# Performance work log

Hardware: AMD Instinct MI355X
Metric: run time of the kernel (lower is better)

Reference implementation:

```python
import jax, jax.numpy as jnp
import numpy as np

EPS = 1e-5

def batchnorm2d(x, w, b):
    # training-mode BN: per-channel stats over (B, H, W), biased variance
    mean = jnp.mean(x, axis=(0, 2, 3), keepdims=True)
    var = jnp.var(x, axis=(0, 2, 3), keepdims=True)
    xn = (x - mean) * jax.lax.rsqrt(var + EPS)
    return xn * w[None, :, None, None] + b[None, :, None, None]

def setup_inputs() -> dict:
    key = jax.random.key(0)
    ks = jax.random.split(key, 12)
    B, C, H, W = 4, 64, 64, 64
    Cq = C // 8
    s = 1.0 / np.sqrt(C)
    return {
        "x": jax.random.normal(ks[0], (B, C, H, W), jnp.float32),
        "Wq": jax.random.normal(ks[1], (Cq, C), jnp.float32) * s,
        "bq": jnp.zeros((Cq,), jnp.float32),
        "Wk": jax.random.normal(ks[2], (Cq, C), jnp.float32) * s,
        "bk": jnp.zeros((Cq,), jnp.float32),
        "Wv": jax.random.normal(ks[3], (C, C), jnp.float32) * s,
        "bv": jnp.zeros((C,), jnp.float32),
        "gamma_p": jax.random.normal(ks[4], (), jnp.float32) * 0.1,
        "bnp_w": jnp.ones((C,), jnp.float32),
        "bnp_b": jnp.zeros((C,), jnp.float32),
        "gamma_c": jax.random.normal(ks[5], (), jnp.float32) * 0.1,
        "bnc_w": jnp.ones((C,), jnp.float32),
        "bnc_b": jnp.zeros((C,), jnp.float32),
    }

def reference(x, Wq, bq, Wk, bk, Wv, bv, gamma_p, bnp_w, bnp_b, gamma_c, bnc_w, bnc_b):
    B, C, H, W = x.shape
    N = H * W
    xf = x.reshape(B, C, N)

    # ---- PAM (position attention) ----
    q = jnp.einsum('dc,bcn->bnd', Wq, xf) + bq  # [B, N, Cq]
    k = jnp.einsum('dc,bcn->bdn', Wk, xf) + bk[None, :, None]  # [B, Cq, N]
    v = jnp.einsum('dc,bcn->bdn', Wv, xf) + bv[None, :, None]  # [B, C, N]
    energy = jnp.einsum('bnd,bdm->bnm', q, k)  # [B, N, N]
    attn = jax.nn.softmax(energy, axis=-1)
    # out[b,c,m] = sum_n v[b,c,n] * attn[m,n]  (bmm(v, attn^T))
    out = jnp.einsum('bcn,bmn->bcm', v, attn).reshape(B, C, H, W)
    out = gamma_p * out
    out = batchnorm2d(out, bnp_w, bnp_b)
    y = out + x  # PAM residual

    # ---- CAM (channel attention) ----
    yf = y.reshape(B, C, N)
    energy_c = jnp.einsum('bcn,bdn->bcd', yf, yf)  # [B, C, C]
    energy_new = jnp.max(energy_c, axis=-1, keepdims=True) - energy_c
    attn_c = jax.nn.softmax(energy_new, axis=-1)
    out_c = jnp.einsum('bcd,bdn->bcn', attn_c, yf).reshape(B, C, H, W)
    out_c = gamma_c * out_c
    out_c = batchnorm2d(out_c, bnc_w, bnc_b)
    return out_c + y  # CAM residual
```

## Files before the change

kernel.cpp:

```cpp
#include <hip/hip_runtime.h>

#define NN 4096
#define EPS 1e-5f

#define Q_OFF   0u
#define K_OFF   131072u
#define V_OFF   262144u
#define O_OFF   1310720u
#define Y_OFF   2359296u
#define OC_OFF  3407872u
#define AT_OFF  4456448u
#define S2_OFF  4472832u
#define PS_OFF  4472960u
#define OP_OFF  4473088u

__global__ __launch_bounds__(256) void proj_kernel(
    const float* __restrict__ x, const float* __restrict__ Wq, const float* __restrict__ bq,
    const float* __restrict__ Wk, const float* __restrict__ bk,
    const float* __restrict__ Wv, const float* __restrict__ bv,
    float* __restrict__ q, float* __restrict__ k, float* __restrict__ v) {
  __shared__ float sWq[8*64], sWk[8*64], sWv[64*64], sbq[8], sbk[8], sbv[64];
  int t = threadIdx.x;
  for (int i = t; i < 512; i += 256) { sWq[i] = Wq[i]; sWk[i] = Wk[i]; }
  for (int i = t; i < 4096; i += 256) sWv[i] = Wv[i];
  if (t < 64) sbv[t] = bv[t];
  if (t < 8) { sbq[t] = bq[t]; sbk[t] = bk[t]; }
  __syncthreads();
  int b = blockIdx.x >> 6;
  int n = ((blockIdx.x & 63) << 6) | (t & 63);
  int cg_ = t >> 6;
  float xv[64];
  #pragma unroll
  for (int c = 0; c < 64; ++c) xv[c] = x[(((b<<6)|c)<<12) | n];
  for (int c = cg_*16; c < cg_*16+16; ++c) {
    float acc = sbv[c];
    #pragma unroll
    for (int c2 = 0; c2 < 64; ++c2) acc += sWv[c*64 + c2] * xv[c2];
    v[(((b<<6)|c)<<12) | n] = acc;
  }
  if (cg_ == 0) {
    #pragma unroll
    for (int d = 0; d < 8; ++d) {
      float acc = sbq[d];
      #pragma unroll
      for (int c = 0; c < 64; ++c) acc += sWq[d*64+c] * xv[c];
      q[(((b<<12)|n)<<3) | d] = acc;
    }
  } else if (cg_ == 1) {
    #pragma unroll
    for (int d = 0; d < 8; ++d) {
      float acc = sbk[d];
      #pragma unroll
      for (int c = 0; c < 64; ++c) acc += sWk[d*64+c] * xv[c];
      k[(((b<<3)|d)<<12) | n] = acc;
    }
  }
}

__global__ __launch_bounds__(256, 4) void attn_kernel(
    const float* __restrict__ q, const float* __restrict__ k,
    const float* __restrict__ v, float* __restrict__ op,
    float* __restrict__ lp, int gsh) {
  __shared__ float kst[64*12];
  __shared__ float vst[64*68];
  __shared__ float pst[64*68];

  const int G    = 1 << gsh;
  const int g    = blockIdx.x & (G - 1);
  const int rest = blockIdx.x >> gsh;
  const int mt   = rest & 63;
  const int b    = rest >> 6;
  const int m0   = mt << 6;
  const int t    = threadIdx.x;

  const int rq = t & 15;
  const int sg = t >> 4;

  float4 qa[4][2];
  #pragma unroll
  for (int r = 0; r < 4; ++r) {
    const float4* qp = (const float4*)&q[(size_t)(((b<<12) | (m0 + (rq<<2) + r)) << 3)];
    qa[r][0] = qp[0]; qa[r][1] = qp[1];
  }

  float lsum[4] = {0.f, 0.f, 0.f, 0.f};
  float av[4][4] = {{0.f}};

  const int span = NN >> gsh;
  const int nbeg = g * span;

  for (int n0 = nbeg; n0 < nbeg + span; n0 += 64) {
    __syncthreads();
    #pragma unroll
    for (int i = t; i < 512; i += 256) {
      int ni = i & 63, d = i >> 6;
      kst[ni*12 + d] = k[(((b<<3)|d)<<12) + n0 + ni];
    }
    #pragma unroll
    for (int i = t; i < 4096; i += 256) {
      int ni = i & 63, c = i >> 6;
      vst[ni*68 + c] = v[(((b<<6)|c)<<12) + n0 + ni];
    }
    __syncthreads();
    #pragma unroll
    for (int j = 0; j < 4; ++j) {
      const int ni = (sg << 2) | j;
      const float4 ka = *(const float4*)&kst[ni*12];
      const float4 kb = *(const float4*)&kst[ni*12 + 4];
      float pj[4];
      #pragma unroll
      for (int r = 0; r < 4; ++r) {
        float s = qa[r][0].x*ka.x + qa[r][0].y*ka.y + qa[r][0].z*ka.z + qa[r][0].w*ka.w
                + qa[r][1].x*kb.x + qa[r][1].y*kb.y + qa[r][1].z*kb.z + qa[r][1].w*kb.w;
        float e = __expf(s);
        pj[r] = e;
        lsum[r] += e;
      }
      *(float4*)&pst[ni*68 + (rq<<2)] = make_float4(pj[0], pj[1], pj[2], pj[3]);
    }
    __syncthreads();
    #pragma unroll 4
    for (int ni = 0; ni < 64; ++ni) {
      const float4 p4 = *(const float4*)&pst[ni*68 + (sg<<2)];
      const float4 v4 = *(const float4*)&vst[ni*68 + (rq<<2)];
      av[0][0] += p4.x*v4.x; av[0][1] += p4.x*v4.y; av[0][2] += p4.x*v4.z; av[0][3] += p4.x*v4.w;
      av[1][0] += p4.y*v4.x; av[1][1] += p4.y*v4.y; av[1][2] += p4.y*v4.z; av[1][3] += p4.y*v4.w;
      av[2][0] += p4.z*v4.x; av[2][1] += p4.z*v4.y; av[2][2] += p4.z*v4.z; av[2][3] += p4.z*v4.w;
      av[3][0] += p4.w*v4.x; av[3][1] += p4.w*v4.y; av[3][2] += p4.w*v4.z; av[3][3] += p4.w*v4.w;
    }
  }
  __syncthreads();
  *(float4*)&pst[sg*68 + (rq<<2)] = make_float4(lsum[0], lsum[1], lsum[2], lsum[3]);
  __syncthreads();
  if (t < 64) {
    float l = 0.f;
    #pragma unroll
    for (int s = 0; s < 16; ++s) l += pst[s*68 + t];
    lp[(((((g<<2)|b)<<6) | mt)<<6) | t] = l;
  }
  float* ob = op + ((size_t)((((g<<2)|b)<<6) | mt) << 12);
  #pragma unroll
  for (int r = 0; r < 4; ++r)
    *(float4*)&ob[((((sg<<2)|r)<<6) | (rq<<2))] =
        make_float4(av[r][0], av[r][1], av[r][2], av[r][3]);
}

__global__ __launch_bounds__(256) void merge_kernel(
    const float* __restrict__ op, const float* __restrict__ lp,
    float* __restrict__ o, float* __restrict__ psums, int G) {
  __shared__ float sm[64*65];
  __shared__ float linv[64];
  const int b = blockIdx.x >> 6, mt = blockIdx.x & 63;
  const int t = threadIdx.x;
  if (t < 64) {
    float l = 0.f;
    for (int g = 0; g < G; ++g)
      l += lp[(((((g<<2)|b)<<6) | mt)<<6) | t];
    linv[t] = 1.f / l;
  }
  __syncthreads();
  for (int i = 0; i < 16; ++i) {
    int idx = (i<<8) + t;
    float s = 0.f;
    for (int g = 0; g < G; ++g)
      s += op[((size_t)((((g<<2)|b)<<6) | mt) << 12) + idx];
    int m = idx >> 6, c = idx & 63;
    sm[c*65 + m] = s * linv[m];
  }
  __syncthreads();
  for (int i = 0; i < 16; ++i) {
    int idx = (i<<8) + t;
    int m = idx & 63, c = idx >> 6;
    float ov = sm[c*65 + m];
    o[(((b<<6)|c)<<12) | (mt<<6) | m] = ov;
    float s1 = ov, s2 = ov*ov;
    #pragma unroll
    for (int off = 32; off; off >>= 1) {
      s1 += __shfl_xor(s1, off, 64);
      s2 += __shfl_xor(s2, off, 64);
    }
    if ((t & 63) == 0) { atomicAdd(&psums[c], s1); atomicAdd(&psums[64+c], s2); }
  }
}

__global__ __launch_bounds__(256) void yg_kernel(
    const float* __restrict__ o, const float* __restrict__ x,
    const float* __restrict__ psums,
    const float* __restrict__ gp, const float* __restrict__ w1, const float* __restrict__ bb1,
    float* __restrict__ y, float* __restrict__ gpart) {
  __shared__ float yt[64*68];
  __shared__ float cf[128];
  const int bi = blockIdx.x;
  const int b = bi >> 6, sp = bi & 63;
  const int t = threadIdx.x;
  const int n0 = sp << 6;
  if (t < 64) {
    float m1 = psums[t] * (1.f/16384.f), m2 = psums[64+t] * (1.f/16384.f);
    float var = m2 - m1*m1;
    float gg = *gp;
    float r = rsqrtf(gg*gg*var + EPS);
    float a = gg * r * w1[t];
    cf[t] = a; cf[64+t] = bb1[t] - m1*a;
  }
  __syncthreads();
  #pragma unroll
  for (int i = 0; i < 16; ++i) {
    int idx = (i<<8) + t;
    int c = idx >> 6, m = idx & 63;
    size_t gi = ((size_t)(((b<<6)|c)<<12)) + n0 + m;
    float yv = o[gi]*cf[c] + cf[64+c] + x[gi];
    yt[c*68 + m] = yv;
    y[gi] = yv;
  }
  __syncthreads();
  {
    int tc = t >> 4, td = t & 15;
    float acc[4][4] = {{0.f}};
    #pragma unroll
    for (int mj = 0; mj < 16; ++mj) {
      float4 ya[4], yb[4];
      #pragma unroll
      for (int r = 0; r < 4; ++r)  ya[r] = *(const float4*)&yt[((tc<<2)+r)*68 + (mj<<2)];
      #pragma unroll
      for (int ss = 0; ss < 4; ++ss) yb[ss] = *(const float4*)&yt[((td<<2)+ss)*68 + (mj<<2)];
      #pragma unroll
      for (int r = 0; r < 4; ++r)
        #pragma unroll
        for (int ss = 0; ss < 4; ++ss)
          acc[r][ss] += ya[r].x*yb[ss].x + ya[r].y*yb[ss].y + ya[r].z*yb[ss].z + ya[r].w*yb[ss].w;
    }
    float* gb = gpart + ((size_t)bi << 12);
    #pragma unroll
    for (int r = 0; r < 4; ++r)
      *(float4*)&gb[(((tc<<2)+r)<<6) | (td<<2)] =
          make_float4(acc[r][0], acc[r][1], acc[r][2], acc[r][3]);
  }
}

__global__ __launch_bounds__(256) void csm_kernel(
    const float* __restrict__ gpart, float* __restrict__ attnc) {
  __shared__ float red[256];
  const int bi = blockIdx.x;
  const int b = bi >> 6, row = bi & 63;
  const int t = threadIdx.x;
  const int d = t & 63, spg = t >> 6;
  float e = 0.f;
  #pragma unroll
  for (int j = 0; j < 16; ++j) {
    int spp = (spg<<4) + j;
    e += gpart[((size_t)((b<<6)|spp) << 12) + (row<<6) + d];
  }
  red[t] = e;
  __syncthreads();
  if (t < 64) {
    float ee = red[t]+red[64+t]+red[128+t]+red[192+t];
    float mn = ee;
    #pragma unroll
    for (int off = 32; off; off >>= 1) mn = fminf(mn, __shfl_xor(mn, off, 64));
    float p = __expf(mn - ee);
    float s = p;
    #pragma unroll
    for (int off = 32; off; off >>= 1) s += __shfl_xor(s, off, 64);
    attnc[(((b<<6)|row)<<6) | t] = p / s;
  }
}

__global__ __launch_bounds__(256) void cam_apply_kernel(
    const float* __restrict__ attn, const float* __restrict__ y,
    float* __restrict__ oc, float* __restrict__ sums) {
  __shared__ float satt[64*68];
  int b = blockIdx.x >> 6;
  int n = ((blockIdx.x & 63) << 6) | (threadIdx.x & 63);
  int cg_ = threadIdx.x >> 6;
  for (int i = threadIdx.x; i < 4096; i += 256)
    satt[(i>>6)*68 + (i&63)] = attn[(b<<12) | i];
  __syncthreads();
  float yv[64];
  #pragma unroll
  for (int d = 0; d < 64; ++d) yv[d] = y[(((b<<6)|d)<<12) | n];
  for (int c = cg_*16; c < cg_*16+16; ++c) {
    float acc = 0.f;
    #pragma unroll
    for (int d4 = 0; d4 < 16; ++d4) {
      float4 avv = *(const float4*)&satt[c*68 + (d4<<2)];
      acc += avv.x*yv[d4*4] + avv.y*yv[d4*4+1] + avv.z*yv[d4*4+2] + avv.w*yv[d4*4+3];
    }
    oc[(((b<<6)|c)<<12) | n] = acc;
    float s1 = acc, s2 = acc*acc;
    #pragma unroll
    for (int off = 32; off; off >>= 1) { s1 += __shfl_xor(s1, off, 64); s2 += __shfl_xor(s2, off, 64); }
    if ((threadIdx.x & 63) == 0) { atomicAdd(&sums[c], s1); atomicAdd(&sums[64+c], s2); }
  }
}

__global__ __launch_bounds__(256) void fin_kernel(
    const float* __restrict__ oc, const float* __restrict__ y,
    const float* __restrict__ s2b,
    const float* __restrict__ gc, const float* __restrict__ w2, const float* __restrict__ bb2,
    float* __restrict__ out) {
  __shared__ float cf[128];
  const int bi = blockIdx.x;
  const int b = bi >> 6, sp = bi & 63;
  const int t = threadIdx.x;
  const int n0 = sp << 6;
  if (t < 64) {
    float m1 = s2b[t] * (1.f/16384.f), m2 = s2b[64+t] * (1.f/16384.f);
    float var = m2 - m1*m1;
    float gg = *gc;
    float r = rsqrtf(gg*gg*var + EPS);
    float a = gg * r * w2[t];
    cf[t] = a; cf[64+t] = bb2[t] - m1*a;
  }
  __syncthreads();
  const int n = t & 63, cg_ = t >> 6;
  #pragma unroll
  for (int j = 0; j < 16; ++j) {
    int c = (cg_<<4) + j;
    size_t gi = ((size_t)(((b<<6)|c)<<12)) + n0 + n;
    out[gi] = oc[gi]*cf[c] + cf[64+c] + y[gi];
  }
}

extern "C" void kernel_launch(void* const* d_in, const int* in_sizes, int n_in,
                              void* d_out, int out_size, void* d_ws, size_t ws_size,
                              hipStream_t stream) {
  (void)in_sizes; (void)n_in; (void)out_size;
  const float* x      = (const float*)d_in[0];
  const float* Wq     = (const float*)d_in[1];
  const float* bq     = (const float*)d_in[2];
  const float* Wk     = (const float*)d_in[3];
  const float* bk     = (const float*)d_in[4];
  const float* Wv     = (const float*)d_in[5];
  const float* bv     = (const float*)d_in[6];
  const float* gp     = (const float*)d_in[7];
  const float* bnp_w  = (const float*)d_in[8];
  const float* bnp_b  = (const float*)d_in[9];
  const float* gc     = (const float*)d_in[10];
  const float* bnc_w  = (const float*)d_in[11];
  const float* bnc_b  = (const float*)d_in[12];

  float* ws = (float*)d_ws;
  float* q   = ws + Q_OFF;
  float* k   = ws + K_OFF;
  float* v   = ws + V_OFF;
  float* o   = ws + O_OFF;
  float* y   = ws + Y_OFF;
  float* oc  = ws + OC_OFF;
  float* atc = ws + AT_OFF;
  float* s2b = ws + S2_OFF;
  float* ps  = ws + PS_OFF;
  float* op  = ws + OP_OFF;
  float* gpart = op;

  int gsh = 0;
  if (ws_size >= 34931712ull)      gsh = 2;
  else if (ws_size >= 26412032ull) gsh = 1;
  const int G = 1 << gsh;
  float* lpart = op + (size_t)G * 1048576u;

  hipMemsetAsync(s2b, 0, 256u * sizeof(float), stream);

  proj_kernel<<<256, 256, 0, stream>>>(x, Wq, bq, Wk, bk, Wv, bv, q, k, v);
  attn_kernel<<<256 << gsh, 256, 0, stream>>>(q, k, v, op, lpart, gsh);
  merge_kernel<<<256, 256, 0, stream>>>(op, lpart, o, ps, G);
  yg_kernel<<<256, 256, 0, stream>>>(o, x, ps, gp, bnp_w, bnp_b, y, gpart);
  csm_kernel<<<256, 256, 0, stream>>>(gpart, atc);
  cam_apply_kernel<<<256, 256, 0, stream>>>(atc, y, oc, s2b);
  fin_kernel<<<256, 256, 0, stream>>>(oc, y, s2b, gc, bnc_w, bnc_b, (float*)d_out);
}
```

Before: 521.0 us.

## Split attention key range across four waves in-block and fuse merge into attn

The attention kernel now runs 1024 threads per block, with four 256-thread groups each covering a quarter of the key positions. Their partial outputs and softmax denominators are reduced through shared memory, and the block then normalises, writes o and accumulates the BN statistics itself. This removes the separate merge kernel and the global partial-sum buffers, which cuts a launch and a round trip through global memory. The projection kernel also stages x through shared memory with float4 loads. The cost is only 256 blocks with one 1024-thread block per CU, so occupancy and per-thread register budget change, and the extra __syncthreads now span the whole block.

```diff
diff --git a/kernel.cpp b/kernel.cpp
--- a/kernel.cpp
+++ b/kernel.cpp
@@ -12,7 +12,7 @@
 #define AT_OFF  4456448u
 #define S2_OFF  4472832u
 #define PS_OFF  4472960u
-#define OP_OFF  4473088u
+#define GP_OFF  4473088u
 
 __global__ __launch_bounds__(256) void proj_kernel(
     const float* __restrict__ x, const float* __restrict__ Wq, const float* __restrict__ bq,
@@ -20,18 +20,27 @@
     const float* __restrict__ Wv, const float* __restrict__ bv,
     float* __restrict__ q, float* __restrict__ k, float* __restrict__ v) {
   __shared__ float sWq[8*64], sWk[8*64], sWv[64*64], sbq[8], sbk[8], sbv[64];
+  __shared__ float xt[64*68];
   int t = threadIdx.x;
+  int b = blockIdx.x >> 6;
+  int sp = blockIdx.x & 63;
+  int n0 = sp << 6;
   for (int i = t; i < 512; i += 256) { sWq[i] = Wq[i]; sWk[i] = Wk[i]; }
   for (int i = t; i < 4096; i += 256) sWv[i] = Wv[i];
   if (t < 64) sbv[t] = bv[t];
   if (t < 8) { sbq[t] = bq[t]; sbk[t] = bk[t]; }
-  __syncthreads();
-  int b = blockIdx.x >> 6;
-  int n = ((blockIdx.x & 63) << 6) | (t & 63);
+  for (int i = t; i < 1024; i += 256) {
+    int c = i >> 4, nf = (i & 15) << 2;
+    *(float4*)&xt[c*68 + nf] =
+        *(const float4*)&x[(size_t)(((b<<6)|c)<<12) + n0 + nf];
+  }
+  __syncthreads();
+  int nl = t & 63;
+  int n = n0 | nl;
   int cg_ = t >> 6;
   float xv[64];
   #pragma unroll
-  for (int c = 0; c < 64; ++c) xv[c] = x[(((b<<6)|c)<<12) | n];
+  for (int c = 0; c < 64; ++c) xv[c] = xt[c*68 + nl];
   for (int c = cg_*16; c < cg_*16+16; ++c) {
     float acc = sbv[c];
     #pragma unroll
@@ -57,24 +66,21 @@
   }
 }
 
-__global__ __launch_bounds__(256, 4) void attn_kernel(
+__global__ __launch_bounds__(1024, 1) void attn_kernel(
     const float* __restrict__ q, const float* __restrict__ k,
-    const float* __restrict__ v, float* __restrict__ op,
-    float* __restrict__ lp, int gsh) {
-  __shared__ float kst[64*12];
-  __shared__ float vst[64*68];
-  __shared__ float pst[64*68];
-
-  const int G    = 1 << gsh;
-  const int g    = blockIdx.x & (G - 1);
-  const int rest = blockIdx.x >> gsh;
-  const int mt   = rest & 63;
-  const int b    = rest >> 6;
-  const int m0   = mt << 6;
-  const int t    = threadIdx.x;
-
-  const int rq = t & 15;
-  const int sg = t >> 4;
+    const float* __restrict__ v, float* __restrict__ o,
+    float* __restrict__ psums) {
+  __shared__ float kst[4][64*12];
+  __shared__ float vst[4][64*68];
+  __shared__ float pst[4][64*68];
+
+  const int b  = blockIdx.x >> 6;
+  const int m0 = (blockIdx.x & 63) << 6;
+  const int t  = threadIdx.x;
+  const int h  = t >> 8;
+  const int u  = t & 255;
+  const int rq = u & 15;
+  const int sg = u >> 4;
 
   float4 qa[4][2];
   #pragma unroll
@@ -86,27 +92,24 @@
   float lsum[4] = {0.f, 0.f, 0.f, 0.f};
   float av[4][4] = {{0.f}};
 
-  const int span = NN >> gsh;
-  const int nbeg = g * span;
-
-  for (int n0 = nbeg; n0 < nbeg + span; n0 += 64) {
+  for (int n0 = h << 6; n0 < NN; n0 += 256) {
     __syncthreads();
     #pragma unroll
-    for (int i = t; i < 512; i += 256) {
+    for (int i = u; i < 512; i += 256) {
       int ni = i & 63, d = i >> 6;
-      kst[ni*12 + d] = k[(((b<<3)|d)<<12) + n0 + ni];
-    }
-    #pragma unroll
-    for (int i = t; i < 4096; i += 256) {
+      kst[h][ni*12 + d] = k[(((b<<3)|d)<<12) + n0 + ni];
+    }
+    #pragma unroll
+    for (int i = u; i < 4096; i += 256) {
       int ni = i & 63, c = i >> 6;
-      vst[ni*68 + c] = v[(((b<<6)|c)<<12) + n0 + ni];
+      vst[h][ni*68 + c] = v[(((b<<6)|c)<<12) + n0 + ni];
     }
     __syncthreads();
     #pragma unroll
     for (int j = 0; j < 4; ++j) {
       const int ni = (sg << 2) | j;
-      const float4 ka = *(const float4*)&kst[ni*12];
-      const float4 kb = *(const float4*)&kst[ni*12 + 4];
+      const float4 ka = *(const float4*)&kst[h][ni*12];
+      const float4 kb = *(const float4*)&kst[h][ni*12 + 4];
       float pj[4];
       #pragma unroll
       for (int r = 0; r < 4; ++r) {
@@ -116,13 +119,13 @@
         pj[r] = e;
         lsum[r] += e;
       }
-      *(float4*)&pst[ni*68 + (rq<<2)] = make_float4(pj[0], pj[1], pj[2], pj[3]);
+      *(float4*)&pst[h][ni*68 + (rq<<2)] = make_float4(pj[0], pj[1], pj[2], pj[3]);
     }
     __syncthreads();
     #pragma unroll 4
     for (int ni = 0; ni < 64; ++ni) {
-      const float4 p4 = *(const float4*)&pst[ni*68 + (sg<<2)];
-      const float4 v4 = *(const float4*)&vst[ni*68 + (rq<<2)];
+      const float4 p4 = *(const float4*)&pst[h][ni*68 + (sg<<2)];
+      const float4 v4 = *(const float4*)&vst[h][ni*68 + (rq<<2)];
       av[0][0] += p4.x*v4.x; av[0][1] += p4.x*v4.y; av[0][2] += p4.x*v4.z; av[0][3] += p4.x*v4.w;
       av[1][0] += p4.y*v4.x; av[1][1] += p4.y*v4.y; av[1][2] += p4.y*v4.z; av[1][3] += p4.y*v4.w;
       av[2][0] += p4.z*v4.x; av[2][1] += p4.z*v4.y; av[2][2] += p4.z*v4.z; av[2][3] += p4.z*v4.w;
@@ -130,56 +133,68 @@
     }
   }
   __syncthreads();
-  *(float4*)&pst[sg*68 + (rq<<2)] = make_float4(lsum[0], lsum[1], lsum[2], lsum[3]);
+  if (h > 0) {
+    float* pav = pst[h];
+    #pragma unroll
+    for (int r = 0; r < 4; ++r)
+      #pragma unroll
+      for (int cc = 0; cc < 4; ++cc)
+        pav[(u<<4) + (r<<2) + cc] = av[r][cc];
+    float* plv = vst[h];
+    #pragma unroll
+    for (int r = 0; r < 4; ++r) plv[(u<<2) + r] = lsum[r];
+  }
+  __syncthreads();
+  if (h == 0) {
+    #pragma unroll
+    for (int qq = 1; qq < 4; ++qq) {
+      #pragma unroll
+      for (int r = 0; r < 4; ++r) {
+        #pragma unroll
+        for (int cc = 0; cc < 4; ++cc)
+          av[r][cc] += pst[qq][(u<<4) + (r<<2) + cc];
+        lsum[r] += vst[qq][(u<<2) + r];
+      }
+    }
+    *(float4*)&pst[0][sg*68 + (rq<<2)] = make_float4(lsum[0], lsum[1], lsum[2], lsum[3]);
+  }
   __syncthreads();
   if (t < 64) {
     float l = 0.f;
     #pragma unroll
-    for (int s = 0; s < 16; ++s) l += pst[s*68 + t];
-    lp[(((((g<<2)|b)<<6) | mt)<<6) | t] = l;
-  }
-  float* ob = op + ((size_t)((((g<<2)|b)<<6) | mt) << 12);
-  #pragma unroll
-  for (int r = 0; r < 4; ++r)
-    *(float4*)&ob[((((sg<<2)|r)<<6) | (rq<<2))] =
-        make_float4(av[r][0], av[r][1], av[r][2], av[r][3]);
-}
-
-__global__ __launch_bounds__(256) void merge_kernel(
-    const float* __restrict__ op, const float* __restrict__ lp,
-    float* __restrict__ o, float* __restrict__ psums, int G) {
-  __shared__ float sm[64*65];
-  __shared__ float linv[64];
-  const int b = blockIdx.x >> 6, mt = blockIdx.x & 63;
-  const int t = threadIdx.x;
-  if (t < 64) {
-    float l = 0.f;
-    for (int g = 0; g < G; ++g)
-      l += lp[(((((g<<2)|b)<<6) | mt)<<6) | t];
-    linv[t] = 1.f / l;
-  }
-  __syncthreads();
-  for (int i = 0; i < 16; ++i) {
-    int idx = (i<<8) + t;
-    float s = 0.f;
-    for (int g = 0; g < G; ++g)
-      s += op[((size_t)((((g<<2)|b)<<6) | mt) << 12) + idx];
-    int m = idx >> 6, c = idx & 63;
-    sm[c*65 + m] = s * linv[m];
-  }
-  __syncthreads();
-  for (int i = 0; i < 16; ++i) {
-    int idx = (i<<8) + t;
-    int m = idx & 63, c = idx >> 6;
-    float ov = sm[c*65 + m];
-    o[(((b<<6)|c)<<12) | (mt<<6) | m] = ov;
-    float s1 = ov, s2 = ov*ov;
-    #pragma unroll
-    for (int off = 32; off; off >>= 1) {
-      s1 += __shfl_xor(s1, off, 64);
-      s2 += __shfl_xor(s2, off, 64);
-    }
-    if ((t & 63) == 0) { atomicAdd(&psums[c], s1); atomicAdd(&psums[64+c], s2); }
+    for (int s = 0; s < 16; ++s) l += pst[0][s*68 + t];
+    kst[0][t] = 1.f / l;
+  }
+  __syncthreads();
+  if (h == 0) {
+    float* sm = vst[0];
+    #pragma unroll
+    for (int r = 0; r < 4; ++r) {
+      const int m = (sg<<2) + r;
+      const float inv = kst[0][m];
+      #pragma unroll
+      for (int cc = 0; cc < 4; ++cc)
+        sm[((rq<<2)+cc)*65 + m] = av[r][cc] * inv;
+    }
+  }
+  __syncthreads();
+  {
+    const int mloc = t & 63;
+    const int wv = t >> 6;
+    const float* sm = vst[0];
+    #pragma unroll
+    for (int it = 0; it < 4; ++it) {
+      const int c = (it<<4) + wv;
+      float ov = sm[c*65 + mloc];
+      o[(size_t)(((b<<6)|c)<<12) + m0 + mloc] = ov;
+      float s1 = ov, s2 = ov*ov;
+      #pragma unroll
+      for (int off = 32; off; off >>= 1) {
+        s1 += __shfl_xor(s1, off, 64);
+        s2 += __shfl_xor(s2, off, 64);
+      }
+      if ((t & 63) == 0) { atomicAdd(&psums[c], s1); atomicAdd(&psums[64+c], s2); }
+    }
   }
 }
 
@@ -324,7 +339,7 @@
 extern "C" void kernel_launch(void* const* d_in, const int* in_sizes, int n_in,
                               void* d_out, int out_size, void* d_ws, size_t ws_size,
                               hipStream_t stream) {
-  (void)in_sizes; (void)n_in; (void)out_size;
+  (void)in_sizes; (void)n_in; (void)out_size; (void)ws_size;
   const float* x      = (const float*)d_in[0];
   const float* Wq     = (const float*)d_in[1];
   const float* bq     = (const float*)d_in[2];
@@ -340,29 +355,21 @@
   const float* bnc_b  = (const float*)d_in[12];
 
   float* ws = (float*)d_ws;
-  float* q   = ws + Q_OFF;
-  float* k   = ws + K_OFF;
-  float* v   = ws + V_OFF;
-  float* o   = ws + O_OFF;
-  float* y   = ws + Y_OFF;
-  float* oc  = ws + OC_OFF;
-  float* atc = ws + AT_OFF;
-  float* s2b = ws + S2_OFF;
-  float* ps  = ws + PS_OFF;
-  float* op  = ws + OP_OFF;
-  float* gpart = op;
-
-  int gsh = 0;
-  if (ws_size >= 34931712ull)      gsh = 2;
-  else if (ws_size >= 26412032ull) gsh = 1;
-  const int G = 1 << gsh;
-  float* lpart = op + (size_t)G * 1048576u;
+  float* q     = ws + Q_OFF;
+  float* k     = ws + K_OFF;
+  float* v     = ws + V_OFF;
+  float* o     = ws + O_OFF;
+  float* y     = ws + Y_OFF;
+  float* oc    = ws + OC_OFF;
+  float* atc   = ws + AT_OFF;
+  float* s2b   = ws + S2_OFF;
+  float* ps    = ws + PS_OFF;
+  float* gpart = ws + GP_OFF;
 
   hipMemsetAsync(s2b, 0, 256u * sizeof(float), stream);
 
   proj_kernel<<<256, 256, 0, stream>>>(x, Wq, bq, Wk, bk, Wv, bv, q, k, v);
-  attn_kernel<<<256 << gsh, 256, 0, stream>>>(q, k, v, op, lpart, gsh);
-  merge_kernel<<<256, 256, 0, stream>>>(op, lpart, o, ps, G);
+  attn_kernel<<<256, 1024, 0, stream>>>(q, k, v, o, ps);
   yg_kernel<<<256, 256, 0, stream>>>(o, x, ps, gp, bnp_w, bnp_b, y, gpart);
   csm_kernel<<<256, 256, 0, stream>>>(gpart, atc);
   cam_apply_kernel<<<256, 256, 0, stream>>>(atc, y, oc, s2b);
```

After: 524.9 us. No clear change (+0.8%).

## Fuse split-K merge into attention via last-block-done counters; stage x tile in LDS

Applied to the files above, without the earlier changes.

The separate merge kernel is folded into the attention kernel. Each of the four key-range blocks for a query tile increments an atomic counter, and the last one to arrive sums the partial outputs and softmax denominators, writes o, and accumulates the BN statistics. The split factor is now fixed at 4 instead of being chosen from the workspace size, and the memset is widened so it also clears the counters. The projection kernel also loads its x tile into shared memory with float4 reads. This removes one kernel launch and its dependency gap, at the cost of a serial tail in the last-arriving block and threadfence overhead.

```diff
diff --git a/kernel.cpp b/kernel.cpp
--- a/kernel.cpp
+++ b/kernel.cpp
@@ -12,7 +12,9 @@
 #define AT_OFF  4456448u
 #define S2_OFF  4472832u
 #define PS_OFF  4472960u
-#define OP_OFF  4473088u
+#define CNT_OFF 4473088u
+#define OP_OFF  4473344u
+#define LP_OFF  8667648u
 
 __global__ __launch_bounds__(256) void proj_kernel(
     const float* __restrict__ x, const float* __restrict__ Wq, const float* __restrict__ bq,
@@ -20,18 +22,27 @@
     const float* __restrict__ Wv, const float* __restrict__ bv,
     float* __restrict__ q, float* __restrict__ k, float* __restrict__ v) {
   __shared__ float sWq[8*64], sWk[8*64], sWv[64*64], sbq[8], sbk[8], sbv[64];
+  __shared__ float xt[64*68];
   int t = threadIdx.x;
+  int b = blockIdx.x >> 6;
+  int sp = blockIdx.x & 63;
+  int n0 = sp << 6;
   for (int i = t; i < 512; i += 256) { sWq[i] = Wq[i]; sWk[i] = Wk[i]; }
   for (int i = t; i < 4096; i += 256) sWv[i] = Wv[i];
   if (t < 64) sbv[t] = bv[t];
   if (t < 8) { sbq[t] = bq[t]; sbk[t] = bk[t]; }
-  __syncthreads();
-  int b = blockIdx.x >> 6;
-  int n = ((blockIdx.x & 63) << 6) | (t & 63);
+  for (int i = t; i < 1024; i += 256) {
+    int c = i >> 4, nf = (i & 15) << 2;
+    *(float4*)&xt[c*68 + nf] =
+        *(const float4*)&x[(size_t)(((b<<6)|c)<<12) + n0 + nf];
+  }
+  __syncthreads();
+  int nl = t & 63;
+  int n = n0 | nl;
   int cg_ = t >> 6;
   float xv[64];
   #pragma unroll
-  for (int c = 0; c < 64; ++c) xv[c] = x[(((b<<6)|c)<<12) | n];
+  for (int c = 0; c < 64; ++c) xv[c] = xt[c*68 + nl];
   for (int c = cg_*16; c < cg_*16+16; ++c) {
     float acc = sbv[c];
     #pragma unroll
@@ -60,14 +71,16 @@
 __global__ __launch_bounds__(256, 4) void attn_kernel(
     const float* __restrict__ q, const float* __restrict__ k,
     const float* __restrict__ v, float* __restrict__ op,
-    float* __restrict__ lp, int gsh) {
+    float* __restrict__ lp, float* __restrict__ o,
+    float* __restrict__ psums, int* __restrict__ cnt) {
   __shared__ float kst[64*12];
   __shared__ float vst[64*68];
   __shared__ float pst[64*68];
-
-  const int G    = 1 << gsh;
-  const int g    = blockIdx.x & (G - 1);
-  const int rest = blockIdx.x >> gsh;
+  __shared__ int who;
+
+  const int bi   = blockIdx.x;
+  const int g    = bi & 3;
+  const int rest = bi >> 2;
   const int mt   = rest & 63;
   const int b    = rest >> 6;
   const int m0   = mt << 6;
@@ -86,7 +99,7 @@
   float lsum[4] = {0.f, 0.f, 0.f, 0.f};
   float av[4][4] = {{0.f}};
 
-  const int span = NN >> gsh;
+  const int span = NN >> 2;
   const int nbeg = g * span;
 
   for (int n0 = nbeg; n0 < nbeg + span; n0 += 64) {
@@ -143,27 +156,33 @@
   for (int r = 0; r < 4; ++r)
     *(float4*)&ob[((((sg<<2)|r)<<6) | (rq<<2))] =
         make_float4(av[r][0], av[r][1], av[r][2], av[r][3]);
-}
-
-__global__ __launch_bounds__(256) void merge_kernel(
-    const float* __restrict__ op, const float* __restrict__ lp,
-    float* __restrict__ o, float* __restrict__ psums, int G) {
-  __shared__ float sm[64*65];
-  __shared__ float linv[64];
-  const int b = blockIdx.x >> 6, mt = blockIdx.x & 63;
-  const int t = threadIdx.x;
+
+  __syncthreads();
+  if (t == 0) {
+    __threadfence();
+    who = atomicAdd(&cnt[(b<<6) | mt], 1);
+  }
+  __syncthreads();
+  if (who != 3) return;
+  if (t == 0) __threadfence();
+  __syncthreads();
+
+  float* sm = vst;
+  float* linv = kst;
   if (t < 64) {
     float l = 0.f;
-    for (int g = 0; g < G; ++g)
-      l += lp[(((((g<<2)|b)<<6) | mt)<<6) | t];
+    #pragma unroll
+    for (int g2 = 0; g2 < 4; ++g2)
+      l += lp[(((((g2<<2)|b)<<6) | mt)<<6) | t];
     linv[t] = 1.f / l;
   }
   __syncthreads();
   for (int i = 0; i < 16; ++i) {
     int idx = (i<<8) + t;
     float s = 0.f;
-    for (int g = 0; g < G; ++g)
-      s += op[((size_t)((((g<<2)|b)<<6) | mt) << 12) + idx];
+    #pragma unroll
+    for (int g2 = 0; g2 < 4; ++g2)
+      s += op[((size_t)((((g2<<2)|b)<<6) | mt) << 12) + idx];
     int m = idx >> 6, c = idx & 63;
     sm[c*65 + m] = s * linv[m];
   }
@@ -246,8 +265,8 @@
   const int d = t & 63, spg = t >> 6;
   float e = 0.f;
   #pragma unroll
-  for (int j = 0; j < 16; ++j) {
-    int spp = (spg<<4) + j;
+  for (int jj = 0; jj < 16; ++jj) {
+    int spp = (spg<<4) + jj;
     e += gpart[((size_t)((b<<6)|spp) << 12) + (row<<6) + d];
   }
   red[t] = e;
@@ -314,8 +333,8 @@
   __syncthreads();
   const int n = t & 63, cg_ = t >> 6;
   #pragma unroll
-  for (int j = 0; j < 16; ++j) {
-    int c = (cg_<<4) + j;
+  for (int jj = 0; jj < 16; ++jj) {
+    int c = (cg_<<4) + jj;
     size_t gi = ((size_t)(((b<<6)|c)<<12)) + n0 + n;
     out[gi] = oc[gi]*cf[c] + cf[64+c] + y[gi];
   }
@@ -324,7 +343,7 @@
 extern "C" void kernel_launch(void* const* d_in, const int* in_sizes, int n_in,
                               void* d_out, int out_size, void* d_ws, size_t ws_size,
                               hipStream_t stream) {
-  (void)in_sizes; (void)n_in; (void)out_size;
+  (void)in_sizes; (void)n_in; (void)out_size; (void)ws_size;
   const float* x      = (const float*)d_in[0];
   const float* Wq     = (const float*)d_in[1];
   const float* bq     = (const float*)d_in[2];
@@ -340,29 +359,24 @@
   const float* bnc_b  = (const float*)d_in[12];
 
   float* ws = (float*)d_ws;
-  float* q   = ws + Q_OFF;
-  float* k   = ws + K_OFF;
-  float* v   = ws + V_OFF;
-  float* o   = ws + O_OFF;
-  float* y   = ws + Y_OFF;
-  float* oc  = ws + OC_OFF;
-  float* atc = ws + AT_OFF;
-  float* s2b = ws + S2_OFF;
-  float* ps  = ws + PS_OFF;
-  float* op  = ws + OP_OFF;
+  float* q     = ws + Q_OFF;
+  float* k     = ws + K_OFF;
+  float* v     = ws + V_OFF;
+  float* o     = ws + O_OFF;
+  float* y     = ws + Y_OFF;
+  float* oc    = ws + OC_OFF;
+  float* atc   = ws + AT_OFF;
+  float* s2b   = ws + S2_OFF;
+  float* ps    = ws + PS_OFF;
+  int*   cnt   = (int*)(ws + CNT_OFF);
+  float* op    = ws + OP_OFF;
+  float* lpart = ws + LP_OFF;
   float* gpart = op;
 
-  int gsh = 0;
-  if (ws_size >= 34931712ull)      gsh = 2;
-  else if (ws_size >= 26412032ull) gsh = 1;
-  const int G = 1 << gsh;
-  float* lpart = op + (size_t)G * 1048576u;
-
-  hipMemsetAsync(s2b, 0, 256u * sizeof(float), stream);
+  hipMemsetAsync(s2b, 0, 512u * sizeof(float), stream);
 
   proj_kernel<<<256, 256, 0, stream>>>(x, Wq, bq, Wk, bk, Wv, bv, q, k, v);
-  attn_kernel<<<256 << gsh, 256, 0, stream>>>(q, k, v, op, lpart, gsh);
-  merge_kernel<<<256, 256, 0, stream>>>(op, lpart, o, ps, G);
+  attn_kernel<<<1024, 256, 0, stream>>>(q, k, v, op, lpart, o, ps, cnt);
   yg_kernel<<<256, 256, 0, stream>>>(o, x, ps, gp, bnp_w, bnp_b, y, gpart);
   csm_kernel<<<256, 256, 0, stream>>>(gpart, atc);
   cam_apply_kernel<<<256, 256, 0, stream>>>(atc, y, oc, s2b);
```

After: 492.7 us. 1.06x faster.
